# Kernel optimization log

Measured on AMD Instinct MI355X. Metric: run time of the kernel, lower is better.

Reference implementation:

```python
import jax, jax.numpy as jnp
import numpy as np

B, H, W = 4, 64, 64
DIM, NH, HD = 768, 12, 64
MLP_DIM = 3072
WS = 14
EPS = 1e-6
SCALE = HD ** -0.5
QMIN, QMAX = -128.0, 127.0  # 8-bit signed fake-quant range


def fake_quant(x, s):
    # uniform quant-dequant with straight-through estimator
    q = jnp.clip(jnp.round(x / s), QMIN, QMAX) * s
    return x + jax.lax.stop_gradient(q - x)


def layer_norm(x, w, b):
    mu = jnp.mean(x, axis=-1, keepdims=True)
    var = jnp.var(x, axis=-1, keepdims=True)
    return (x - mu) * jax.lax.rsqrt(var + EPS) * w + b


def qlinear(x, w, b, a_s, w_s):
    # PreQuantizedLayer: fake-quant input activation and weight, then linear
    return fake_quant(x, a_s) @ fake_quant(w, w_s).T + b


def _attention(xw, qkv_w, qkv_b, proj_w, proj_b, rel_pos_h, rel_pos_w, a_s, w_s):
    Bw = xw.shape[0]
    N = WS * WS
    qkv = qlinear(xw.reshape(Bw, N, DIM), qkv_w, qkv_b, a_s[4], w_s[0])
    qkv = qkv.reshape(Bw, N, 3, NH, HD).transpose(2, 0, 3, 1, 4).reshape(3, Bw * NH, N, HD)
    q = fake_quant(qkv[0], a_s[0])
    k = fake_quant(qkv[1], a_s[1])
    v = fake_quant(qkv[2], a_s[2])
    attn = jnp.einsum('bqc,bkc->bqk', q * SCALE, k)  # (Bw*NH, N, N)
    # decomposed relative position bias (q_size == k_size == WS)
    idx = jnp.arange(WS)[:, None] - jnp.arange(WS)[None, :] + (WS - 1)
    Rh = rel_pos_h[idx]  # (WS, WS, HD)
    Rw = rel_pos_w[idx]
    r_q = q.reshape(Bw * NH, WS, WS, HD)
    rel_h = jnp.einsum('bhwc,hkc->bhwk', r_q, Rh)
    rel_w = jnp.einsum('bhwc,wkc->bhwk', r_q, Rw)
    attn = (attn.reshape(-1, WS, WS, WS, WS) + rel_h[..., :, None] + rel_w[..., None, :]).reshape(-1, N, N)
    attn = fake_quant(jax.nn.softmax(attn, axis=-1), a_s[3])
    out = jnp.einsum('bqk,bkc->bqc', attn, v)
    out = out.reshape(Bw, NH, WS, WS, HD).transpose(0, 2, 3, 1, 4).reshape(Bw, WS, WS, DIM)
    return qlinear(out, proj_w, proj_b, a_s[5], w_s[1])


def _forward(x, ln1_w, ln1_b, ln2_w, ln2_b, qkv_w, qkv_b, proj_w, proj_b,
             lin1_w, lin1_b, lin2_w, lin2_b, rel_pos_h, rel_pos_w, act_scales, w_scales):
    shortcut = x
    h = layer_norm(x, ln1_w, ln1_b)
    pad_h = (WS - H % WS) % WS
    pad_w = (WS - W % WS) % WS
    Hp, Wp = H + pad_h, W + pad_w
    hp = jnp.pad(h, ((0, 0), (0, pad_h), (0, pad_w), (0, 0)))
    win = hp.reshape(B, Hp // WS, WS, Wp // WS, WS, DIM).transpose(0, 1, 3, 2, 4, 5).reshape(-1, WS, WS, DIM)
    win = _attention(win, qkv_w, qkv_b, proj_w, proj_b, rel_pos_h, rel_pos_w, act_scales, w_scales)
    hp = win.reshape(B, Hp // WS, Wp // WS, WS, WS, DIM).transpose(0, 1, 3, 2, 4, 5).reshape(B, Hp, Wp, DIM)
    x = shortcut + hp[:, :H, :W, :]
    y = layer_norm(x, ln2_w, ln2_b)
    y = qlinear(y, lin1_w, lin1_b, act_scales[6], w_scales[2])
    y = jax.nn.gelu(y, approximate=False)
    y = qlinear(y, lin2_w, lin2_b, act_scales[7], w_scales[3])
    return x + y


def setup_inputs() -> dict:
    key = jax.random.key(0)
    ks = jax.random.split(key, 12)
    def w(k, shape, std=0.02):
        return jax.random.normal(k, shape, dtype=jnp.float32) * std
    return {
        'x': jax.random.normal(ks[0], (B, H, W, DIM), dtype=jnp.float32),
        'ln1_w': jnp.ones((DIM,), jnp.float32), 'ln1_b': jnp.zeros((DIM,), jnp.float32),
        'ln2_w': jnp.ones((DIM,), jnp.float32), 'ln2_b': jnp.zeros((DIM,), jnp.float32),
        'qkv_w': w(ks[1], (3 * DIM, DIM)), 'qkv_b': jnp.zeros((3 * DIM,), jnp.float32),
        'proj_w': w(ks[2], (DIM, DIM)), 'proj_b': jnp.zeros((DIM,), jnp.float32),
        'lin1_w': w(ks[3], (MLP_DIM, DIM)), 'lin1_b': jnp.zeros((MLP_DIM,), jnp.float32),
        'lin2_w': w(ks[4], (DIM, MLP_DIM)), 'lin2_b': jnp.zeros((DIM,), jnp.float32),
        'rel_pos_h': w(ks[5], (2 * WS - 1, HD)), 'rel_pos_w': w(ks[6], (2 * WS - 1, HD)),
        'act_scales': jax.random.uniform(ks[7], (8,), jnp.float32, 0.01, 0.06),
        'w_scales': jax.random.uniform(ks[8], (4,), jnp.float32, 0.0005, 0.003),
    }


def reference(x, ln1_w, ln1_b, ln2_w, ln2_b, qkv_w, qkv_b, proj_w, proj_b,
              lin1_w, lin1_b, lin2_w, lin2_b, rel_pos_h, rel_pos_w, act_scales, w_scales):
    return _forward(x, ln1_w, ln1_b, ln2_w, ln2_b, qkv_w, qkv_b, proj_w, proj_b,
                    lin1_w, lin1_b, lin2_w, lin2_b, rel_pos_h, rel_pos_w, act_scales, w_scales)
```

## Files before the change

### kernel.cpp

```cpp
#include <hip/hip_runtime.h>
#include <cstdint>


typedef int   v4i __attribute__((ext_vector_type(4)));
typedef float v4f __attribute__((ext_vector_type(4)));
typedef short v8s __attribute__((ext_vector_type(8)));
typedef int8_t i8;

__device__ __forceinline__ i8 satq(float x) {
  float q = rintf(x);
  q = fminf(127.f, fmaxf(-128.f, q));
  return (i8)(int)q;
}

__device__ __forceinline__ void gload16(const i8* g, i8* l) {
  __builtin_amdgcn_global_load_lds((const __attribute__((address_space(1))) void*)g,
                                   (__attribute__((address_space(3))) void*)l, 16, 0, 0);
}

__device__ __forceinline__ int pack4(const i8* q) {
  return ((int)(unsigned char)q[0]) | ((int)(unsigned char)q[1] << 8) |
         ((int)(unsigned char)q[2] << 16) | ((int)(unsigned char)q[3] << 24);
}

__device__ __forceinline__ float fast_gelu(float v) {
  float x = fabsf(v) * 0.70710678118654752f;
  float t = __builtin_amdgcn_rcpf(fmaf(0.3275911f, x, 1.0f));
  float s = fmaf(1.061405429f, t, -1.453152027f);
  s = fmaf(s, t, 1.421413741f);
  s = fmaf(s, t, -0.284496736f);
  s = fmaf(s, t, 0.254829592f);
  s = s * t;
  float e = __expf(-x * x);
  float erfa = fmaf(-s, e, 1.0f);
  float erfs = copysignf(erfa, v);
  float hv = 0.5f * v;
  return fmaf(hv, erfs, hv);
}

__global__ __launch_bounds__(256) void k_prep(const float* __restrict__ qkvw,
    const float* __restrict__ projw, const float* __restrict__ lin1w,
    const float* __restrict__ lin2w, i8* __restrict__ wqb,
    const float* __restrict__ rph, const float* __restrict__ rpw,
    short* __restrict__ TB, const float* __restrict__ wsc) {
  int b = blockIdx.x;
  if (b < 1728) {
    int i = b * 256 + threadIdx.x;
    const float* w; int base, sidx;
    if (i < 110592)      { w = qkvw;  base = 0;      sidx = 0; }
    else if (i < 147456) { w = projw; base = 110592; sidx = 1; }
    else if (i < 294912) { w = lin1w; base = 147456; sidx = 2; }
    else                 { w = lin2w; base = 294912; sidx = 3; }
    float inv = 1.0f / wsc[sidx];
    const float4* src = (const float4*)w + (size_t)(i - base) * 4;
    i8 buf[16];
#pragma unroll
    for (int t = 0; t < 4; t++) {
      float4 f = src[t];
      buf[t*4+0] = satq(f.x * inv); buf[t*4+1] = satq(f.y * inv);
      buf[t*4+2] = satq(f.z * inv); buf[t*4+3] = satq(f.w * inv);
    }
    *(v4i*)(wqb + (size_t)i * 16) = *(v4i*)buf;
  } else {
    int g = (b - 1728) * 256 + threadIdx.x;
    int lane = g & 63, c = g >> 6;
    int p = c & 1, ks = (c >> 1) & 1, nt = (c >> 2) & 1, tb = c >> 3;
    const float* src = tb ? rpw : rph;
    int n = nt * 16 + (lane & 15);
    int k0 = ks * 32 + (lane >> 4) * 8;
    short outv[8];
#pragma unroll
    for (int j = 0; j < 8; j++) {
      float v = (n < 27) ? src[n * 64 + k0 + j] : 0.f;
      unsigned u = __float_as_uint(v);
      unsigned hi = (u + 0x7fffu + ((u >> 16) & 1u)) >> 16;
      if (p == 0) outv[j] = (short)hi;
      else {
        float lof = v - __uint_as_float(hi << 16);
        unsigned ul = __float_as_uint(lof);
        outv[j] = (short)((ul + 0x7fffu + ((ul >> 16) & 1u)) >> 16);
      }
    }
    *(v8s*)(TB + (size_t)c * 512 + lane * 8) = *(v8s*)outv;
  }
}

__global__ __launch_bounds__(256) void k_ln1(const float* __restrict__ x,
    const float* __restrict__ w, const float* __restrict__ b,
    const float* __restrict__ as, i8* __restrict__ outq) {
  int wt = blockIdx.x * 4 + (threadIdx.x >> 6);
  int lane = threadIdx.x & 63;
  int win = wt / 196, tok = wt - win * 196;
  int bb = win / 25, wrem = win - bb * 25, wh = wrem / 5, ww = wrem - wh * 5;
  int r = tok / 14, c = tok - r * 14;
  int y = wh * 14 + r, xx = ww * 14 + c;
  i8* dst = outq + (size_t)wt * 768 + lane * 12;
  if (y >= 64 || xx >= 64) {
    ((int*)dst)[0] = 0; ((int*)dst)[1] = 0; ((int*)dst)[2] = 0;
    return;
  }
  const float* row = x + (((size_t)bb * 64 + y) * 64 + xx) * 768 + lane * 12;
  float v[12];
  *(float4*)(v)     = *(const float4*)(row);
  *(float4*)(v + 4) = *(const float4*)(row + 4);
  *(float4*)(v + 8) = *(const float4*)(row + 8);
  float s = 0.f, ss = 0.f;
#pragma unroll
  for (int j = 0; j < 12; j++) { s += v[j]; ss += v[j] * v[j]; }
#pragma unroll
  for (int off = 1; off < 64; off <<= 1) { s += __shfl_xor(s, off); ss += __shfl_xor(ss, off); }
  float mu = s * (1.0f / 768.0f);
  float var = ss * (1.0f / 768.0f) - mu * mu;
  float rstd = 1.0f / sqrtf(var + 1e-6f);
  float inv = 1.0f / as[4];
  float wv[12], bv[12];
  *(float4*)(wv)     = *(const float4*)(w + lane * 12);
  *(float4*)(wv + 4) = *(const float4*)(w + lane * 12 + 4);
  *(float4*)(wv + 8) = *(const float4*)(w + lane * 12 + 8);
  *(float4*)(bv)     = *(const float4*)(b + lane * 12);
  *(float4*)(bv + 4) = *(const float4*)(b + lane * 12 + 4);
  *(float4*)(bv + 8) = *(const float4*)(b + lane * 12 + 8);
  i8 q[12];
#pragma unroll
  for (int j = 0; j < 12; j++) q[j] = satq(((v[j] - mu) * rstd * wv[j] + bv[j]) * inv);
  ((int*)dst)[0] = pack4(q); ((int*)dst)[1] = pack4(q + 4); ((int*)dst)[2] = pack4(q + 8);
}

__global__ __launch_bounds__(256) void k_ln2(const float* __restrict__ x2,
    const float* __restrict__ w, const float* __restrict__ b,
    const float* __restrict__ as, i8* __restrict__ outq) {
  int tokg = blockIdx.x * 4 + (threadIdx.x >> 6);
  int lane = threadIdx.x & 63;
  const float* row = x2 + (size_t)tokg * 768 + lane * 12;
  float v[12];
  *(float4*)(v)     = *(const float4*)(row);
  *(float4*)(v + 4) = *(const float4*)(row + 4);
  *(float4*)(v + 8) = *(const float4*)(row + 8);
  float s = 0.f, ss = 0.f;
#pragma unroll
  for (int j = 0; j < 12; j++) { s += v[j]; ss += v[j] * v[j]; }
#pragma unroll
  for (int off = 1; off < 64; off <<= 1) { s += __shfl_xor(s, off); ss += __shfl_xor(ss, off); }
  float mu = s * (1.0f / 768.0f);
  float var = ss * (1.0f / 768.0f) - mu * mu;
  float rstd = 1.0f / sqrtf(var + 1e-6f);
  float inv = 1.0f / as[6];
  float wv[12], bv[12];
  *(float4*)(wv)     = *(const float4*)(w + lane * 12);
  *(float4*)(wv + 4) = *(const float4*)(w + lane * 12 + 4);
  *(float4*)(wv + 8) = *(const float4*)(w + lane * 12 + 8);
  *(float4*)(bv)     = *(const float4*)(b + lane * 12);
  *(float4*)(bv + 4) = *(const float4*)(b + lane * 12 + 4);
  *(float4*)(bv + 8) = *(const float4*)(b + lane * 12 + 8);
  i8* dst = outq + (size_t)tokg * 768 + lane * 12;
  i8 q[12];
#pragma unroll
  for (int j = 0; j < 12; j++) q[j] = satq(((v[j] - mu) * rstd * wv[j] + bv[j]) * inv);
  ((int*)dst)[0] = pack4(q); ((int*)dst)[1] = pack4(q + 4); ((int*)dst)[2] = pack4(q + 8);
}

template <class Epi, bool AHEAD = false>
__global__ __launch_bounds__(256) void k_gemm(const i8* __restrict__ A, const i8* __restrict__ B,
                                              int M, int N, int K, Epi epi) {
  __shared__ __align__(16) i8 As[3][8192];
  __shared__ __align__(16) i8 Bs[3][8192];
  const int tid = threadIdx.x;
  const int lane = tid & 63, wave = tid >> 6;
  const int quad = lane >> 4, lc = lane & 15;
  const int wr = wave >> 1, wc = wave & 1;
  const long bm = (long)blockIdx.y * 128, bn = (long)blockIdx.x * 128;
  const v4i vz = {0, 0, 0, 0};
  v4i acc[4][4];
#pragma unroll
  for (int i = 0; i < 4; i++)
#pragma unroll
    for (int j = 0; j < 4; j++) acc[i][j] = vz;

  const int r0 = tid >> 2, c0 = tid & 3;
  const int cs = c0 ^ ((r0 >> 1) & 3);
  long rA0 = bm + r0;      if (rA0 >= M) rA0 = 0;
  long rA1 = bm + r0 + 64; if (rA1 >= M) rA1 = 0;
  const i8 *pA0, *pA1;
  long astep;
  if (AHEAD) {
    long w0 = rA0 / 196, t0 = rA0 - w0 * 196;
    long w1 = rA1 / 196, t1 = rA1 - w1 * 196;
    pA0 = A + (w0 * 2352 + t0) * 64 + cs * 16;
    pA1 = A + (w1 * 2352 + t1) * 64 + cs * 16;
    astep = 196 * 64;
  } else {
    pA0 = A + rA0 * (size_t)K + cs * 16;
    pA1 = A + rA1 * (size_t)K + cs * 16;
    astep = 64;
  }
  const i8* pB0 = B + (bn + r0)      * (size_t)K + cs * 16;
  const i8* pB1 = B + (bn + r0 + 64) * (size_t)K + cs * 16;

  auto stage = [&](int buf) {
    gload16(pA0, As[buf] + tid * 16); gload16(pA1, As[buf] + 4096 + tid * 16);
    gload16(pB0, Bs[buf] + tid * 16); gload16(pB1, Bs[buf] + 4096 + tid * 16);
    pA0 += astep; pA1 += astep; pB0 += 64; pB1 += 64;
  };

  const int xq16 = (quad ^ ((lc >> 1) & 3)) * 16;

  auto compute = [&](int buf) {
    v4i af[4], bf[4];
#pragma unroll
    for (int i = 0; i < 4; i++) af[i] = *(const v4i*)(As[buf] + (wr * 64 + i * 16 + lc) * 64 + xq16);
#pragma unroll
    for (int j = 0; j < 4; j++) bf[j] = *(const v4i*)(Bs[buf] + (wc * 64 + j * 16 + lc) * 64 + xq16);
#pragma unroll
    for (int i = 0; i < 4; i++)
#pragma unroll
      for (int j = 0; j < 4; j++)
        acc[i][j] = __builtin_amdgcn_mfma_i32_16x16x64_i8(bf[j], af[i], acc[i][j], 0, 0, 0);
  };

  const int nt = K >> 6;
  stage(0); stage(1);
  int cb = 0, sb = 2;
  for (int t = 0; t < nt - 1; ++t) {
    asm volatile("s_waitcnt vmcnt(4)" ::: "memory");
    __builtin_amdgcn_s_barrier();
    asm volatile("" ::: "memory");
    if (t + 2 < nt) { stage(sb); if (++sb == 3) sb = 0; }
    compute(cb); if (++cb == 3) cb = 0;
  }
  asm volatile("s_waitcnt vmcnt(0)" ::: "memory");
  __builtin_amdgcn_s_barrier();
  asm volatile("" ::: "memory");
  compute(cb);

  Epi e = epi;
  e.init();
#pragma unroll
  for (int i = 0; i < 4; i++) {
    int gm = (int)bm + wr * 64 + i * 16 + lc;
#pragma unroll
    for (int j = 0; j < 4; j++) {
      int gn0 = (int)bn + wc * 64 + j * 16 + quad * 4;
      if (gm < M) e.store4(acc[i][j], gm, gn0);
    }
  }
}

struct EpiQKV {
  const float* as; const float* wsc; const float* bias;
  i8 *qq, *kq, *vt;
  float sab, invq, invk, invv;
  __device__ void init() {
    sab = as[4] * wsc[0]; invq = 1.f / as[0]; invk = 1.f / as[1]; invv = 1.f / as[2];
  }
  __device__ void store4(const v4i a, int m, int n0) {
    int t = n0 / 768, rem = n0 - t * 768;
    int head = rem >> 6, ch0 = rem & 63;
    int win = m / 196, tok = m - win * 196;
    size_t bh = (size_t)win * 12 + head;
    float4 bv = *(const float4*)(bias + n0);
    const float* bp = (const float*)&bv;
    if (t == 2) {
#pragma unroll
      for (int r = 0; r < 4; r++)
        vt[(bh * 64 + ch0 + r) * 256 + tok] = satq(((float)a[r] * sab + bp[r]) * invv);
    } else {
      float inv = (t == 0) ? invq : invk;
      i8 q[4];
#pragma unroll
      for (int r = 0; r < 4; r++) q[r] = satq(((float)a[r] * sab + bp[r]) * inv);
      *(int*)((t == 0 ? qq : kq) + (bh * 196 + tok) * 64 + ch0) = pack4(q);
    }
  }
};

struct EpiProj {
  const float* as; const float* wsc; const float* bias; const float* x0; float* out;
  float sab;
  __device__ void init() { sab = as[5] * wsc[1]; }
  __device__ void store4(const v4i a, int m, int n0) {
    int win = m / 196, tok = m - win * 196;
    int bb = win / 25, wrem = win - bb * 25, wh = wrem / 5, ww = wrem - wh * 5;
    int rr = tok / 14, cc = tok - rr * 14;
    int y = wh * 14 + rr, xx = ww * 14 + cc;
    if (y >= 64 || xx >= 64) return;
    size_t o = (((size_t)bb * 64 + y) * 64 + xx) * 768 + n0;
    float4 bv = *(const float4*)(bias + n0);
    float4 xv = *(const float4*)(x0 + o);
    float4 ov;
    ov.x = (float)a[0] * sab + bv.x + xv.x;
    ov.y = (float)a[1] * sab + bv.y + xv.y;
    ov.z = (float)a[2] * sab + bv.z + xv.z;
    ov.w = (float)a[3] * sab + bv.w + xv.w;
    *(float4*)(out + o) = ov;
  }
};

struct EpiLin1 {
  const float* as; const float* wsc; const float* bias; i8* outq;
  float sab, invg;
  __device__ void init() { sab = as[6] * wsc[2]; invg = 1.f / as[7]; }
  __device__ void store4(const v4i a, int m, int n0) {
    float4 bv = *(const float4*)(bias + n0);
    const float* bp = (const float*)&bv;
    i8 q[4];
#pragma unroll
    for (int r = 0; r < 4; r++) {
      float v = fmaf((float)a[r], sab, bp[r]);
      q[r] = satq(fast_gelu(v) * invg);
    }
    *(int*)(outq + (size_t)m * 3072 + n0) = pack4(q);
  }
};

struct EpiLin2 {
  const float* as; const float* wsc; const float* bias; float* out;
  float sab;
  __device__ void init() { sab = as[7] * wsc[3]; }
  __device__ void store4(const v4i a, int m, int n0) {
    size_t o = (size_t)m * 768 + n0;
    float4 bv = *(const float4*)(bias + n0);
    float4 ov = *(const float4*)(out + o);
    ov.x += (float)a[0] * sab + bv.x;
    ov.y += (float)a[1] * sab + bv.y;
    ov.z += (float)a[2] * sab + bv.z;
    ov.w += (float)a[3] * sab + bv.w;
    *(float4*)(out + o) = ov;
  }
};

__global__ __launch_bounds__(64) void k_attn(const i8* __restrict__ qq, const i8* __restrict__ kq,
    const i8* __restrict__ vt, const short* __restrict__ TB,
    const float* __restrict__ as, i8* __restrict__ outq) {
  __shared__ float relS[16][66];
  const int g = blockIdx.x;
  const int work = (g & 7) * 1950 + (g >> 3);
  const int bh = work / 13;
  const int t = work - bh * 13;
  const int lane = threadIdx.x;
  const int quad = lane >> 4, lc = lane & 15;
  const float s0 = as[0];
  const float ssc = s0 * as[1] * 0.125f;
  const float invs3 = 1.0f / as[3];
  const float oscale = as[2] * as[3] / as[5];

  const v8s* TBv = (const v8s*)TB;
  const v4i vz = {0, 0, 0, 0};

  {
    int arow = t * 16 + lc; if (arow > 195) arow = 195;
    const i8* qrow = qq + ((size_t)bh * 196 + arow) * 64;
    v8s af[2];
#pragma unroll
    for (int ks = 0; ks < 2; ks++) {
      const i8* p = qrow + ks * 32 + quad * 8;
#pragma unroll
      for (int j = 0; j < 8; j++)
        af[ks][j] = (short)(__float_as_uint((float)p[j]) >> 16);
    }
    v4f rh0 = {0,0,0,0}, rh1 = {0,0,0,0}, rw0 = {0,0,0,0}, rw1 = {0,0,0,0};
#pragma unroll
    for (int ks = 0; ks < 2; ks++)
#pragma unroll
      for (int p2 = 0; p2 < 2; p2++) {
        rh0 = __builtin_amdgcn_mfma_f32_16x16x32_bf16(af[ks], TBv[(0*4 + ks*2 + p2)*64 + lane], rh0, 0, 0, 0);
        rh1 = __builtin_amdgcn_mfma_f32_16x16x32_bf16(af[ks], TBv[(1*4 + ks*2 + p2)*64 + lane], rh1, 0, 0, 0);
        rw0 = __builtin_amdgcn_mfma_f32_16x16x32_bf16(af[ks], TBv[(2*4 + ks*2 + p2)*64 + lane], rw0, 0, 0, 0);
        rw1 = __builtin_amdgcn_mfma_f32_16x16x32_bf16(af[ks], TBv[(3*4 + ks*2 + p2)*64 + lane], rw1, 0, 0, 0);
      }
#pragma unroll
    for (int r = 0; r < 4; r++) {
      int rl = quad * 4 + r;
      relS[rl][lc]      = rh0[r] * s0;
      relS[rl][16 + lc] = rh1[r] * s0;
      relS[rl][32 + lc] = rw0[r] * s0;
      relS[rl][48 + lc] = rw1[r] * s0;
    }
  }

  v4i aq = *(const v4i*)(qq + ((size_t)bh * 196 + t * 16 + lc) * 64 + quad * 16);
  v4i sacc[13];
#pragma unroll
  for (int f = 0; f < 13; f++) {
    v4i bk = *(const v4i*)(kq + ((size_t)bh * 196 + f * 16 + lc) * 64 + quad * 16);
    sacc[f] = __builtin_amdgcn_mfma_i32_16x16x64_i8(bk, aq, vz, 0, 0, 0);
  }

  unsigned khw[13];
#pragma unroll
  for (int f = 0; f < 13; f++) {
    unsigned w0 = 0, w1 = 0, w2 = 0, w3 = 0;
#pragma unroll
    for (int r = 0; r < 4; r++) {
      int k0 = f*16 + 0*4 + r; if (k0 > 195) k0 = 195;
      int k1 = f*16 + 1*4 + r; if (k1 > 195) k1 = 195;
      int k2 = f*16 + 2*4 + r; if (k2 > 195) k2 = 195;
      int k3 = f*16 + 3*4 + r; if (k3 > 195) k3 = 195;
      w0 |= (unsigned)(((k0/14) << 4) | (k0 - (k0/14)*14)) << (r*8);
      w1 |= (unsigned)(((k1/14) << 4) | (k1 - (k1/14)*14)) << (r*8);
      w2 |= (unsigned)(((k2/14) << 4) | (k2 - (k2/14)*14)) << (r*8);
      w3 |= (unsigned)(((k3/14) << 4) | (k3 - (k3/14)*14)) << (r*8);
    }
    khw[f] = quad == 0 ? w0 : quad == 1 ? w1 : quad == 2 ? w2 : w3;
  }

  int qrow = t * 16 + lc;
  int qh = qrow / 14, qw = qrow - qh * 14;
  const float* rH = &relS[lc][13 + qh];
  const float* rW = &relS[lc][32 + 13 + qw];
  float L[13][4];
  float mx = -1e30f;
#pragma unroll
  for (int f = 0; f < 13; f++)
#pragma unroll
    for (int r = 0; r < 4; r++) {
      int kh = (int)((khw[f] >> (r * 8 + 4)) & 0xfu);
      int kw = (int)((khw[f] >> (r * 8)) & 0xfu);
      float v = ((f < 12) | (quad == 0))
                  ? fmaf((float)sacc[f][r], ssc, rH[-kh] + rW[-kw]) : -1e30f;
      L[f][r] = v;
      mx = fmaxf(mx, v);
    }
  mx = fmaxf(mx, __shfl_xor(mx, 16));
  mx = fmaxf(mx, __shfl_xor(mx, 32));
  float sum = 0.f;
#pragma unroll
  for (int f = 0; f < 13; f++)
#pragma unroll
    for (int r = 0; r < 4; r++) { float e = __expf(L[f][r] - mx); L[f][r] = e; sum += e; }
  sum += __shfl_xor(sum, 16);
  sum += __shfl_xor(sum, 32);
  float cq = (1.0f / sum) * invs3;

  unsigned W[16];
#pragma unroll
  for (int f = 0; f < 13; f++) {
    i8 q4[4];
#pragma unroll
    for (int r = 0; r < 4; r++) q4[r] = satq(L[f][r] * cq);
    W[f] = (unsigned)pack4(q4);
  }
  W[13] = 0; W[14] = 0; W[15] = 0;

  const bool q0m = (quad & 1) == 0, q1m = (quad & 2) == 0;

  v4i oacc[4];
#pragma unroll
  for (int nt = 0; nt < 4; nt++) oacc[nt] = vz;
#pragma unroll
  for (int kc = 0; kc < 4; kc++) {
    unsigned a0 = W[kc*4+0], a1 = W[kc*4+1], a2 = W[kc*4+2], a3 = W[kc*4+3];
    unsigned s0_ = (unsigned)__shfl_xor((int)a1, 16);
    unsigned s1_ = (unsigned)__shfl_xor((int)a0, 16);
    unsigned s2_ = (unsigned)__shfl_xor((int)a3, 16);
    unsigned s3_ = (unsigned)__shfl_xor((int)a2, 16);
    unsigned x0 = q0m ? a0 : s0_;
    unsigned x1 = q0m ? s1_ : a1;
    unsigned x2 = q0m ? a2 : s2_;
    unsigned x3 = q0m ? s3_ : a3;
    unsigned u0 = (unsigned)__shfl_xor((int)x2, 32);
    unsigned u1 = (unsigned)__shfl_xor((int)x3, 32);
    unsigned u2 = (unsigned)__shfl_xor((int)x0, 32);
    unsigned u3 = (unsigned)__shfl_xor((int)x1, 32);
    v4i ap;
    ap[0] = (int)(q1m ? x0 : u0);
    ap[1] = (int)(q1m ? x1 : u1);
    ap[2] = (int)(q1m ? u2 : x2);
    ap[3] = (int)(q1m ? u3 : x3);
#pragma unroll
    for (int nt = 0; nt < 4; nt++) {
      v4i bv = *(const v4i*)(vt + ((size_t)bh * 64 + nt * 16 + lc) * 256 + kc * 64 + quad * 16);
      oacc[nt] = __builtin_amdgcn_mfma_i32_16x16x64_i8(bv, ap, oacc[nt], 0, 0, 0);
    }
  }

  unsigned W2[4];
#pragma unroll
  for (int nt = 0; nt < 4; nt++) {
    i8 q4[4];
#pragma unroll
    for (int r = 0; r < 4; r++) q4[r] = satq((float)oacc[nt][r] * oscale);
    W2[nt] = (unsigned)pack4(q4);
  }
  {
    unsigned a0 = W2[0], a1 = W2[1], a2 = W2[2], a3 = W2[3];
    unsigned s0_ = (unsigned)__shfl_xor((int)a1, 16);
    unsigned s1_ = (unsigned)__shfl_xor((int)a0, 16);
    unsigned s2_ = (unsigned)__shfl_xor((int)a3, 16);
    unsigned s3_ = (unsigned)__shfl_xor((int)a2, 16);
    unsigned x0 = q0m ? a0 : s0_;
    unsigned x1 = q0m ? s1_ : a1;
    unsigned x2 = q0m ? a2 : s2_;
    unsigned x3 = q0m ? s3_ : a3;
    unsigned u0 = (unsigned)__shfl_xor((int)x2, 32);
    unsigned u1 = (unsigned)__shfl_xor((int)x3, 32);
    unsigned u2 = (unsigned)__shfl_xor((int)x0, 32);
    unsigned u3 = (unsigned)__shfl_xor((int)x1, 32);
    v4i ot;
    ot[0] = (int)(q1m ? x0 : u0);
    ot[1] = (int)(q1m ? x1 : u1);
    ot[2] = (int)(q1m ? u2 : x2);
    ot[3] = (int)(q1m ? u3 : x3);
    if (t * 16 + lc < 196)
      *(v4i*)(outq + ((size_t)bh * 196 + t * 16 + lc) * 64 + quad * 16) = ot;
  }
}

extern "C" void kernel_launch(void* const* d_in, const int* in_sizes, int n_in,
                              void* d_out, int out_size, void* d_ws, size_t ws_size,
                              hipStream_t stream) {
  const float* x     = (const float*)d_in[0];
  const float* ln1w  = (const float*)d_in[1];
  const float* ln1b  = (const float*)d_in[2];
  const float* ln2w  = (const float*)d_in[3];
  const float* ln2b  = (const float*)d_in[4];
  const float* qkvw  = (const float*)d_in[5];
  const float* qkvb  = (const float*)d_in[6];
  const float* projw = (const float*)d_in[7];
  const float* projb = (const float*)d_in[8];
  const float* lin1w = (const float*)d_in[9];
  const float* lin1b = (const float*)d_in[10];
  const float* lin2w = (const float*)d_in[11];
  const float* lin2b = (const float*)d_in[12];
  const float* rph   = (const float*)d_in[13];
  const float* rpw   = (const float*)d_in[14];
  const float* as    = (const float*)d_in[15];
  const float* wsc   = (const float*)d_in[16];
  float* out = (float*)d_out;

  char* ws = (char*)d_ws;
  i8* big    = (i8*)ws;
  i8* qq     = big;
  i8* kq     = big + 15052800;
  i8* vt     = big + 30105600;
  short* TB  = (short*)(big + 49766400);
  i8* mlpq   = big;
  i8* creg   = (i8*)(ws + 50331648);
  i8* winq   = creg;
  i8* attno  = creg;
  i8* yq     = creg;
  i8* wqb    = (i8*)(ws + 65384448);
  i8* qkvwq  = wqb;
  i8* projwq = wqb + 1769472;
  i8* lin1wq = projwq + 589824;
  i8* lin2wq = lin1wq + 2359296;

  k_prep<<<1732, 256, 0, stream>>>(qkvw, projw, lin1w, lin2w, wqb, rph, rpw, TB, wsc);

  k_ln1<<<4900, 256, 0, stream>>>(x, ln1w, ln1b, as, winq);

  { EpiQKV e{as, wsc, qkvb, qq, kq, vt};
    k_gemm<EpiQKV><<<dim3(18, 154), 256, 0, stream>>>(winq, qkvwq, 19600, 2304, 768, e); }

  k_attn<<<15600, 64, 0, stream>>>(qq, kq, vt, TB, as, attno);

  { EpiProj e{as, wsc, projb, x, out};
    k_gemm<EpiProj, true><<<dim3(6, 154), 256, 0, stream>>>(attno, projwq, 19600, 768, 768, e); }

  k_ln2<<<4096, 256, 0, stream>>>(out, ln2w, ln2b, as, yq);

  { EpiLin1 e{as, wsc, lin1b, mlpq};
    k_gemm<EpiLin1><<<dim3(24, 128), 256, 0, stream>>>(yq, lin1wq, 16384, 3072, 768, e); }

  { EpiLin2 e{as, wsc, lin2b, out};
    k_gemm<EpiLin2><<<dim3(6, 128), 256, 0, stream>>>(mlpq, lin2wq, 16384, 768, 3072, e); }
}
```

Measured before the change: 466.7 us.

## Deepen GEMM LDS pipeline to five stages and merge prep with LN1

The int8 GEMM's shared-memory ring grows from 3 to 5 buffers, with four tiles prefetched ahead and explicit drain steps at the end, to hide more global-load latency. LDS use rises from 48KB to 80KB per block, which may cut occupancy. Separately, the weight-quantization prep kernel and the LN1 kernel are merged into one launch so their blocks run concurrently and one launch is saved. The drain logic assumes K/64 >= 4, which holds for K of 768 and 3072.

```diff
diff --git a/kernel.cpp b/kernel.cpp
--- a/kernel.cpp
+++ b/kernel.cpp
@@ -38,11 +38,14 @@
   return fmaf(hv, erfs, hv);
 }
 
-__global__ __launch_bounds__(256) void k_prep(const float* __restrict__ qkvw,
+__global__ __launch_bounds__(256) void k_prep_ln1(const float* __restrict__ qkvw,
     const float* __restrict__ projw, const float* __restrict__ lin1w,
     const float* __restrict__ lin2w, i8* __restrict__ wqb,
     const float* __restrict__ rph, const float* __restrict__ rpw,
-    short* __restrict__ TB, const float* __restrict__ wsc) {
+    short* __restrict__ TB, const float* __restrict__ wsc,
+    const float* __restrict__ x, const float* __restrict__ ln1w,
+    const float* __restrict__ ln1b, const float* __restrict__ as,
+    i8* __restrict__ winq) {
   int b = blockIdx.x;
   if (b < 1728) {
     int i = b * 256 + threadIdx.x;
@@ -61,7 +64,7 @@
       buf[t*4+2] = satq(f.z * inv); buf[t*4+3] = satq(f.w * inv);
     }
     *(v4i*)(wqb + (size_t)i * 16) = *(v4i*)buf;
-  } else {
+  } else if (b < 1732) {
     int g = (b - 1728) * 256 + threadIdx.x;
     int lane = g & 63, c = g >> 6;
     int p = c & 1, ks = (c >> 1) & 1, nt = (c >> 2) & 1, tb = c >> 3;
@@ -82,48 +85,44 @@
       }
     }
     *(v8s*)(TB + (size_t)c * 512 + lane * 8) = *(v8s*)outv;
-  }
-}
-
-__global__ __launch_bounds__(256) void k_ln1(const float* __restrict__ x,
-    const float* __restrict__ w, const float* __restrict__ b,
-    const float* __restrict__ as, i8* __restrict__ outq) {
-  int wt = blockIdx.x * 4 + (threadIdx.x >> 6);
-  int lane = threadIdx.x & 63;
-  int win = wt / 196, tok = wt - win * 196;
-  int bb = win / 25, wrem = win - bb * 25, wh = wrem / 5, ww = wrem - wh * 5;
-  int r = tok / 14, c = tok - r * 14;
-  int y = wh * 14 + r, xx = ww * 14 + c;
-  i8* dst = outq + (size_t)wt * 768 + lane * 12;
-  if (y >= 64 || xx >= 64) {
-    ((int*)dst)[0] = 0; ((int*)dst)[1] = 0; ((int*)dst)[2] = 0;
-    return;
-  }
-  const float* row = x + (((size_t)bb * 64 + y) * 64 + xx) * 768 + lane * 12;
-  float v[12];
-  *(float4*)(v)     = *(const float4*)(row);
-  *(float4*)(v + 4) = *(const float4*)(row + 4);
-  *(float4*)(v + 8) = *(const float4*)(row + 8);
-  float s = 0.f, ss = 0.f;
-#pragma unroll
-  for (int j = 0; j < 12; j++) { s += v[j]; ss += v[j] * v[j]; }
-#pragma unroll
-  for (int off = 1; off < 64; off <<= 1) { s += __shfl_xor(s, off); ss += __shfl_xor(ss, off); }
-  float mu = s * (1.0f / 768.0f);
-  float var = ss * (1.0f / 768.0f) - mu * mu;
-  float rstd = 1.0f / sqrtf(var + 1e-6f);
-  float inv = 1.0f / as[4];
-  float wv[12], bv[12];
-  *(float4*)(wv)     = *(const float4*)(w + lane * 12);
-  *(float4*)(wv + 4) = *(const float4*)(w + lane * 12 + 4);
-  *(float4*)(wv + 8) = *(const float4*)(w + lane * 12 + 8);
-  *(float4*)(bv)     = *(const float4*)(b + lane * 12);
-  *(float4*)(bv + 4) = *(const float4*)(b + lane * 12 + 4);
-  *(float4*)(bv + 8) = *(const float4*)(b + lane * 12 + 8);
-  i8 q[12];
-#pragma unroll
-  for (int j = 0; j < 12; j++) q[j] = satq(((v[j] - mu) * rstd * wv[j] + bv[j]) * inv);
-  ((int*)dst)[0] = pack4(q); ((int*)dst)[1] = pack4(q + 4); ((int*)dst)[2] = pack4(q + 8);
+  } else {
+    int wt = (b - 1732) * 4 + (threadIdx.x >> 6);
+    int lane = threadIdx.x & 63;
+    int win = wt / 196, tok = wt - win * 196;
+    int bb = win / 25, wrem = win - bb * 25, wh = wrem / 5, ww = wrem - wh * 5;
+    int r = tok / 14, c = tok - r * 14;
+    int y = wh * 14 + r, xx = ww * 14 + c;
+    i8* dst = winq + (size_t)wt * 768 + lane * 12;
+    if (y >= 64 || xx >= 64) {
+      ((int*)dst)[0] = 0; ((int*)dst)[1] = 0; ((int*)dst)[2] = 0;
+      return;
+    }
+    const float* row = x + (((size_t)bb * 64 + y) * 64 + xx) * 768 + lane * 12;
+    float v[12];
+    *(float4*)(v)     = *(const float4*)(row);
+    *(float4*)(v + 4) = *(const float4*)(row + 4);
+    *(float4*)(v + 8) = *(const float4*)(row + 8);
+    float s = 0.f, ss = 0.f;
+#pragma unroll
+    for (int j = 0; j < 12; j++) { s += v[j]; ss += v[j] * v[j]; }
+#pragma unroll
+    for (int off = 1; off < 64; off <<= 1) { s += __shfl_xor(s, off); ss += __shfl_xor(ss, off); }
+    float mu = s * (1.0f / 768.0f);
+    float var = ss * (1.0f / 768.0f) - mu * mu;
+    float rstd = 1.0f / sqrtf(var + 1e-6f);
+    float inv = 1.0f / as[4];
+    float wv[12], bv[12];
+    *(float4*)(wv)     = *(const float4*)(ln1w + lane * 12);
+    *(float4*)(wv + 4) = *(const float4*)(ln1w + lane * 12 + 4);
+    *(float4*)(wv + 8) = *(const float4*)(ln1w + lane * 12 + 8);
+    *(float4*)(bv)     = *(const float4*)(ln1b + lane * 12);
+    *(float4*)(bv + 4) = *(const float4*)(ln1b + lane * 12 + 4);
+    *(float4*)(bv + 8) = *(const float4*)(ln1b + lane * 12 + 8);
+    i8 q[12];
+#pragma unroll
+    for (int j = 0; j < 12; j++) q[j] = satq(((v[j] - mu) * rstd * wv[j] + bv[j]) * inv);
+    ((int*)dst)[0] = pack4(q); ((int*)dst)[1] = pack4(q + 4); ((int*)dst)[2] = pack4(q + 8);
+  }
 }
 
 __global__ __launch_bounds__(256) void k_ln2(const float* __restrict__ x2,
@@ -162,8 +161,8 @@
 template <class Epi, bool AHEAD = false>
 __global__ __launch_bounds__(256) void k_gemm(const i8* __restrict__ A, const i8* __restrict__ B,
                                               int M, int N, int K, Epi epi) {
-  __shared__ __align__(16) i8 As[3][8192];
-  __shared__ __align__(16) i8 Bs[3][8192];
+  __shared__ __align__(16) i8 As[5][8192];
+  __shared__ __align__(16) i8 Bs[5][8192];
   const int tid = threadIdx.x;
   const int lane = tid & 63, wave = tid >> 6;
   const int quad = lane >> 4, lc = lane & 15;
@@ -218,15 +217,23 @@
   };
 
   const int nt = K >> 6;
-  stage(0); stage(1);
-  int cb = 0, sb = 2;
-  for (int t = 0; t < nt - 1; ++t) {
-    asm volatile("s_waitcnt vmcnt(4)" ::: "memory");
+  stage(0); stage(1); stage(2); stage(3);
+  int cb = 0, sb = 4;
+  for (int t = 0; t < nt - 3; ++t) {
+    asm volatile("s_waitcnt vmcnt(12)" ::: "memory");
     __builtin_amdgcn_s_barrier();
     asm volatile("" ::: "memory");
-    if (t + 2 < nt) { stage(sb); if (++sb == 3) sb = 0; }
-    compute(cb); if (++cb == 3) cb = 0;
-  }
+    if (t + 4 < nt) { stage(sb); if (++sb == 5) sb = 0; }
+    compute(cb); if (++cb == 5) cb = 0;
+  }
+  asm volatile("s_waitcnt vmcnt(8)" ::: "memory");
+  __builtin_amdgcn_s_barrier();
+  asm volatile("" ::: "memory");
+  compute(cb); if (++cb == 5) cb = 0;
+  asm volatile("s_waitcnt vmcnt(4)" ::: "memory");
+  __builtin_amdgcn_s_barrier();
+  asm volatile("" ::: "memory");
+  compute(cb); if (++cb == 5) cb = 0;
   asm volatile("s_waitcnt vmcnt(0)" ::: "memory");
   __builtin_amdgcn_s_barrier();
   asm volatile("" ::: "memory");
@@ -544,9 +551,8 @@
   i8* lin1wq = projwq + 589824;
   i8* lin2wq = lin1wq + 2359296;
 
-  k_prep<<<1732, 256, 0, stream>>>(qkvw, projw, lin1w, lin2w, wqb, rph, rpw, TB, wsc);
-
-  k_ln1<<<4900, 256, 0, stream>>>(x, ln1w, ln1b, as, winq);
+  k_prep_ln1<<<6632, 256, 0, stream>>>(qkvw, projw, lin1w, lin2w, wqb,
+                                       rph, rpw, TB, wsc, x, ln1w, ln1b, as, winq);
 
   { EpiQKV e{as, wsc, qkvb, qq, kq, vt};
     k_gemm<EpiQKV><<<dim3(18, 154), 256, 0, stream>>>(winq, qkvwq, 19600, 2304, 768, e); }
```

New measurement: 503.7 us. +7.9%, slower.
